# Kernel optimization log

Hardware: AMD Instinct MI355X
Metric: run time of the kernel (lower is better)

The kernel has to match this reference:

```python
import jax, jax.numpy as jnp
import numpy as np

HIDDEN = 512
SR = 16000
MAX_MSGS = 512
EOT = 2.0  # END_OF_TRACK message-type id (round-to-nearest-even match, like Python round)


def gru_cell(x, h, w_ih, w_hh, b_ih, b_hh):
    # PyTorch GRU cell equations
    gi = w_ih @ x + b_ih          # [3H]
    gh = w_hh @ h + b_hh          # [3H]
    i_r, i_z, i_n = jnp.split(gi, 3)
    h_r, h_z, h_n = jnp.split(gh, 3)
    r = jax.nn.sigmoid(i_r + h_r)
    z = jax.nn.sigmoid(i_z + h_z)
    n = jnp.tanh(i_n + r * h_n)
    return (1.0 - z) * n + z * h


def setup_inputs() -> dict:
    key = jax.random.key(0)
    ks = jax.random.split(key, 8)
    s = 0.02  # keep gates unsaturated
    return {
        "x": jax.random.normal(ks[0], (1, 32, SR), dtype=jnp.float32),
        "enc_w_ih": jax.random.normal(ks[1], (3 * HIDDEN, SR), jnp.float32) * s,
        "enc_w_hh": jax.random.normal(ks[2], (3 * HIDDEN, HIDDEN), jnp.float32) * s,
        "enc_b_ih": jnp.zeros((3 * HIDDEN,), jnp.float32),
        "enc_b_hh": jnp.zeros((3 * HIDDEN,), jnp.float32),
        "dec_w_ih": jax.random.normal(ks[3], (3 * HIDDEN, 6), jnp.float32) * s,
        "dec_w_hh": jax.random.normal(ks[4], (3 * HIDDEN, HIDDEN), jnp.float32) * s,
        "dec_b_ih": jnp.zeros((3 * HIDDEN,), jnp.float32),
        "dec_b_hh": jnp.zeros((3 * HIDDEN,), jnp.float32),
        "lin_w": jax.random.normal(ks[5], (6, HIDDEN), jnp.float32) * s,
        "lin_b": jnp.zeros((6,), jnp.float32),
    }


def _forward(x, enc_w_ih, enc_w_hh, enc_b_ih, enc_b_hh,
             dec_w_ih, dec_w_hh, dec_b_ih, dec_b_hh, lin_w, lin_b):
    # --- encoder: hidden_states[0] in the torch code is the final hidden of
    # encoder layer 0, forward direction (other layers/direction never reach the output).
    xs = x[0]  # [T, SR], batch_size == 1 (required by the original indexing)

    def enc_step(h, xt):
        return gru_cell(xt, h, enc_w_ih, enc_w_hh, enc_b_ih, enc_b_hh), None

    h_enc, _ = jax.lax.scan(enc_step, jnp.zeros((HIDDEN,), x.dtype), xs)

    # --- decoder step 0: zero input, init hidden = h_enc
    h = gru_cell(jnp.zeros((6,), x.dtype), h_enc, dec_w_ih, dec_w_hh, dec_b_ih, dec_b_hh)
    msg0 = lin_w @ h + lin_b
    midi = jnp.zeros((MAX_MSGS, 6), x.dtype).at[0].set(msg0)
    # NOTE: the original never writes midi[:,1] (off-by-one: messages jumps 1 -> 2);
    # torch leaves uninitialized garbage there, we leave zeros.

    def dec_step(carry, _):
        midi, h, last, messages, active = carry
        cond = active & (jnp.round(last[0]) != EOT) & (messages < MAX_MSGS - 1)
        h_new = gru_cell(last, h, dec_w_ih, dec_w_hh, dec_b_ih, dec_b_hh)
        msg = lin_w @ h_new + lin_b
        messages = jnp.where(cond, messages + 1, messages)
        h = jnp.where(cond, h_new, h)
        midi = midi.at[messages].set(jnp.where(cond, msg, midi[messages]))
        last = jnp.where(cond, msg, last)
        return (midi, h, last, messages, cond), None

    init = (midi, h, msg0, jnp.array(1, jnp.int32), jnp.array(True))
    (midi, _, _, messages, _), _ = jax.lax.scan(dec_step, init, None, length=MAX_MSGS - 2)
    num_messages = (messages + 1)[None].astype(jnp.int32)  # torch uses uint32
    return midi[None], num_messages  # ([1, MAX_MSGS, 6], [1])


def reference(x, enc_w_ih, enc_w_hh, enc_b_ih, enc_b_hh,
              dec_w_ih, dec_w_hh, dec_b_ih, dec_b_hh, lin_w, lin_b):
    return _forward(x, enc_w_ih, enc_w_hh, enc_b_ih, enc_b_hh,
                    dec_w_ih, dec_w_hh, dec_b_ih, dec_b_hh, lin_w, lin_b)
```

## Files before the change

kernel.cpp:

```cpp
#include <hip/hip_runtime.h>


#define HID 512
#define G3  1536
#define NWG 16
#define TPB 384
#define JPW 32
#define RPW 96

#define WS_CNT  0
#define WS_HEX  64
#define WS_PMSG 1088
#define WS_GI   4096

__device__ __forceinline__ float sigmf(float x) { return 1.0f / (1.0f + expf(-x)); }

__device__ __forceinline__ void st_agent(float* p, float v) {
  __hip_atomic_store((unsigned int*)p, __float_as_uint(v), __ATOMIC_RELAXED, __HIP_MEMORY_SCOPE_AGENT);
}
__device__ __forceinline__ float ld_agent(const float* p) {
  unsigned int u = __hip_atomic_load((const unsigned int*)p, __ATOMIC_RELAXED, __HIP_MEMORY_SCOPE_AGENT);
  return __uint_as_float(u);
}
__device__ __forceinline__ void ld_agent2(const float* p, float& a, float& b) {
  unsigned long long u = __hip_atomic_load((const unsigned long long*)p, __ATOMIC_RELAXED, __HIP_MEMORY_SCOPE_AGENT);
  a = __uint_as_float((unsigned int)u);
  b = __uint_as_float((unsigned int)(u >> 32));
}

__global__ __launch_bounds__(256) void k0_init(float* __restrict__ ws, float* __restrict__ out,
                                               const float* __restrict__ enc_b_ih) {
  int i = blockIdx.x * 256 + threadIdx.x;
  int n = gridDim.x * 256;
  for (int j = i; j < 4096; j += n) ws[j] = 0.0f;
  for (int j = i; j < 32 * G3; j += n) ws[WS_GI + j] = enc_b_ih[j % G3];
  for (int j = i; j < 3073; j += n) out[j] = 0.0f;
}

#define KB 160
__global__ __launch_bounds__(256) void k1_gemm(const float* __restrict__ x,
                                               const float* __restrict__ wih,
                                               float* __restrict__ ws) {
  __shared__ float lw[64][KB + 4];
  __shared__ float lx[32][KB + 4];
  const int m0  = blockIdx.x * 64;
  const int k00 = blockIdx.y * 1600;
  const int t   = threadIdx.x;
  const int rg  = t >> 4;
  const int tg  = t & 15;
  float acc[4][2] = {{0.f,0.f},{0.f,0.f},{0.f,0.f},{0.f,0.f}};
  for (int c = 0; c < 10; ++c) {
    const int kc = k00 + c * KB;
    __syncthreads();
    #pragma unroll
    for (int j = 0; j < 10; ++j) {
      int idx = t + j * 256;
      int r = idx / 40, c4 = idx % 40;
      float4 v = *reinterpret_cast<const float4*>(wih + (long)(m0 + r) * 16000 + kc + c4 * 4);
      *reinterpret_cast<float4*>(&lw[r][c4 * 4]) = v;
    }
    #pragma unroll
    for (int j = 0; j < 5; ++j) {
      int idx = t + j * 256;
      int r = idx / 40, c4 = idx % 40;
      float4 v = *reinterpret_cast<const float4*>(x + (long)r * 16000 + kc + c4 * 4);
      *reinterpret_cast<float4*>(&lx[r][c4 * 4]) = v;
    }
    __syncthreads();
    for (int kk = 0; kk < KB; kk += 4) {
      float4 xv0 = *reinterpret_cast<const float4*>(&lx[tg * 2 + 0][kk]);
      float4 xv1 = *reinterpret_cast<const float4*>(&lx[tg * 2 + 1][kk]);
      #pragma unroll
      for (int j = 0; j < 4; ++j) {
        float4 wv = *reinterpret_cast<const float4*>(&lw[rg * 4 + j][kk]);
        acc[j][0] += wv.x * xv0.x + wv.y * xv0.y + wv.z * xv0.z + wv.w * xv0.w;
        acc[j][1] += wv.x * xv1.x + wv.y * xv1.y + wv.z * xv1.z + wv.w * xv1.w;
      }
    }
  }
  #pragma unroll
  for (int j = 0; j < 4; ++j)
    #pragma unroll
    for (int u = 0; u < 2; ++u)
      atomicAdd(&ws[WS_GI + (tg * 2 + u) * G3 + m0 + rg * 4 + j], acc[j][u]);
}

__device__ __forceinline__ void load_wslice(const float* __restrict__ whh, int j0, int rg, int cg,
                                            float w[8][16]) {
  #pragma unroll
  for (int k = 0; k < 8; ++k) {
    const int lr = rg * 8 + k;
    const int grow = (lr >> 5) * HID + j0 + (lr & 31);
    const float* src = whh + grow * HID + cg * 16;
    #pragma unroll
    for (int q = 0; q < 4; ++q) {
      float4 v = *reinterpret_cast<const float4*>(src + q * 4);
      w[k][q * 4 + 0] = v.x; w[k][q * 4 + 1] = v.y;
      w[k][q * 4 + 2] = v.z; w[k][q * 4 + 3] = v.w;
    }
  }
}

__global__ __launch_bounds__(TPB) void k2_rnn(
    const float* __restrict__ enc_w_hh, const float* __restrict__ enc_b_hh,
    const float* __restrict__ dec_w_ih, const float* __restrict__ dec_w_hh,
    const float* __restrict__ dec_b_ih, const float* __restrict__ dec_b_hh,
    const float* __restrict__ lin_w, const float* __restrict__ lin_b,
    float* __restrict__ ws, float* __restrict__ out) {
  __shared__ float gsum[RPW];
  __shared__ float h_own[JPW];
  __shared__ float s_last[8];
  __shared__ float s_wih[RPW][6];
  __shared__ float s_bih[RPW];
  __shared__ float s_bhh[RPW];
  __shared__ float s_linw[6][JPW];
  __shared__ float s_linb[6];
  __shared__ float s_pm[NWG][6];

  const int wg = blockIdx.x;
  const int t  = threadIdx.x;
  const int rg = t >> 5;
  const int cg = t & 31;
  const int j0 = wg * JPW;

  unsigned* cnt = (unsigned*)ws;
  float* hex  = ws + WS_HEX;
  float* pmsg = ws + WS_PMSG;
  const float* gi_enc = ws + WS_GI;

  float w[8][16];
  unsigned bstep = 0;
  int p = 0;

  load_wslice(enc_w_hh, j0, rg, cg, w);
  if (t < RPW) {
    const int grow = (t >> 5) * HID + j0 + (t & 31);
    s_bhh[t] = enc_b_hh[grow];
  }
  if (t < JPW) h_own[t] = 0.0f;
  __syncthreads();

  for (int s = 0; s < 32; ++s) {
    float hr[16];
    {
      const float* hb = hex + p * HID + cg * 16;
      #pragma unroll
      for (int u = 0; u < 8; ++u) ld_agent2(hb + 2 * u, hr[2 * u], hr[2 * u + 1]);
    }
    float gi0 = 0.f, gi1 = 0.f, gi2 = 0.f;
    if (t < JPW) {
      const float* g = gi_enc + s * G3 + j0 + t;
      gi0 = g[0]; gi1 = g[HID]; gi2 = g[2 * HID];
    }
    float acc[8];
    #pragma unroll
    for (int k = 0; k < 8; ++k) {
      float a = 0.f;
      #pragma unroll
      for (int i = 0; i < 16; ++i) a = fmaf(w[k][i], hr[i], a);
      acc[k] = a;
    }
    #pragma unroll
    for (int m = 1; m <= 16; m <<= 1) {
      #pragma unroll
      for (int k = 0; k < 8; ++k) acc[k] += __shfl_xor(acc[k], m, 64);
    }
    if (cg == 0) {
      #pragma unroll
      for (int k = 0; k < 8; ++k) gsum[rg * 8 + k] = acc[k];
    }
    __syncthreads();
    if (t < JPW) {
      float r = sigmf(gi0 + gsum[t]      + s_bhh[t]);
      float z = sigmf(gi1 + gsum[32 + t] + s_bhh[32 + t]);
      float n = tanhf(gi2 + r * (gsum[64 + t] + s_bhh[64 + t]));
      float hn = (1.0f - z) * n + z * h_own[t];
      h_own[t] = hn;
      st_agent(&hex[(p ^ 1) * HID + j0 + t], hn);
    }
    p ^= 1;
    ++bstep;
    __syncthreads();
    if (t == 0) {
      __hip_atomic_fetch_add(cnt, 1u, __ATOMIC_ACQ_REL, __HIP_MEMORY_SCOPE_AGENT);
      const unsigned tgt = NWG * bstep;
      while (__hip_atomic_load(cnt, __ATOMIC_ACQUIRE, __HIP_MEMORY_SCOPE_AGENT) < tgt)
        __builtin_amdgcn_s_sleep(1);
    }
    __syncthreads();
  }

  load_wslice(dec_w_hh, j0, rg, cg, w);
  if (t < RPW) {
    const int grow = (t >> 5) * HID + j0 + (t & 31);
    s_bih[t] = dec_b_ih[grow];
    s_bhh[t] = dec_b_hh[grow];
    #pragma unroll
    for (int m = 0; m < 6; ++m) s_wih[t][m] = dec_w_ih[grow * 6 + m];
  }
  if (t < 192) {
    const int m = t >> 5, jj = t & 31;
    s_linw[m][jj] = lin_w[m * HID + j0 + jj];
  }
  if (t < 6) s_linb[t] = lin_b[t];
  __syncthreads();

  int messages = 1;

  for (int k = 0; k <= 510; ++k) {
    if (k >= 1) {
      const bool cond = (rintf(s_last[0]) != 2.0f) && (messages < 511);
      if (!cond) break;
    }
    float hr[16];
    {
      const float* hb = hex + p * HID + cg * 16;
      #pragma unroll
      for (int u = 0; u < 8; ++u) ld_agent2(hb + 2 * u, hr[2 * u], hr[2 * u + 1]);
    }
    float acc[8];
    #pragma unroll
    for (int kk = 0; kk < 8; ++kk) {
      float a = 0.f;
      #pragma unroll
      for (int i = 0; i < 16; ++i) a = fmaf(w[kk][i], hr[i], a);
      acc[kk] = a;
    }
    #pragma unroll
    for (int m = 1; m <= 16; m <<= 1) {
      #pragma unroll
      for (int kk = 0; kk < 8; ++kk) acc[kk] += __shfl_xor(acc[kk], m, 64);
    }
    if (cg == 0) {
      #pragma unroll
      for (int kk = 0; kk < 8; ++kk) gsum[rg * 8 + kk] = acc[kk];
    }
    __syncthreads();
    if (t < JPW) {
      float gi0 = s_bih[t], gi1 = s_bih[32 + t], gi2 = s_bih[64 + t];
      if (k >= 1) {
        #pragma unroll
        for (int m = 0; m < 6; ++m) {
          gi0 = fmaf(s_wih[t][m],      s_last[m], gi0);
          gi1 = fmaf(s_wih[32 + t][m], s_last[m], gi1);
          gi2 = fmaf(s_wih[64 + t][m], s_last[m], gi2);
        }
      }
      float r = sigmf(gi0 + gsum[t]      + s_bhh[t]);
      float z = sigmf(gi1 + gsum[32 + t] + s_bhh[32 + t]);
      float n = tanhf(gi2 + r * (gsum[64 + t] + s_bhh[64 + t]));
      float hn = (1.0f - z) * n + z * h_own[t];
      h_own[t] = hn;
      st_agent(&hex[(p ^ 1) * HID + j0 + t], hn);
    }
    __syncthreads();
    if (t >= 32 && t < 38) {
      const int m = t - 32;
      float pm = 0.f;
      #pragma unroll
      for (int jj = 0; jj < JPW; ++jj) pm = fmaf(s_linw[m][jj], h_own[jj], pm);
      st_agent(&pmsg[(k & 1) * NWG * 8 + wg * 8 + m], pm);
    }
    p ^= 1;
    ++bstep;
    __syncthreads();
    if (t == 0) {
      __hip_atomic_fetch_add(cnt, 1u, __ATOMIC_ACQ_REL, __HIP_MEMORY_SCOPE_AGENT);
      const unsigned tgt = NWG * bstep;
      while (__hip_atomic_load(cnt, __ATOMIC_ACQUIRE, __HIP_MEMORY_SCOPE_AGENT) < tgt)
        __builtin_amdgcn_s_sleep(1);
    }
    __syncthreads();
    if (t >= 128 && t < 128 + NWG * 6) {
      const int wi = (t - 128) / 6, m = (t - 128) % 6;
      s_pm[wi][m] = ld_agent(&pmsg[(k & 1) * NWG * 8 + wi * 8 + m]);
    }
    __syncthreads();
    if (t < 6) {
      float sme = s_linb[t];
      #pragma unroll
      for (int wi = 0; wi < NWG; ++wi) sme += s_pm[wi][t];
      s_last[t] = sme;
      if (wg == 0) {
        const int row = (k == 0) ? 0 : (messages + 1);
        out[row * 6 + t] = sme;
      }
    }
    __syncthreads();
    if (k >= 1) ++messages;
  }

  if (wg == 0 && t == 0) out[3072] = (float)(messages + 1);
}

extern "C" void kernel_launch(void* const* d_in, const int* in_sizes, int n_in,
                              void* d_out, int out_size, void* d_ws, size_t ws_size,
                              hipStream_t stream) {
  const float* x        = (const float*)d_in[0];
  const float* enc_w_ih = (const float*)d_in[1];
  const float* enc_w_hh = (const float*)d_in[2];
  const float* enc_b_ih = (const float*)d_in[3];
  const float* enc_b_hh = (const float*)d_in[4];
  const float* dec_w_ih = (const float*)d_in[5];
  const float* dec_w_hh = (const float*)d_in[6];
  const float* dec_b_ih = (const float*)d_in[7];
  const float* dec_b_hh = (const float*)d_in[8];
  const float* lin_w    = (const float*)d_in[9];
  const float* lin_b    = (const float*)d_in[10];
  float* ws  = (float*)d_ws;
  float* out = (float*)d_out;

  hipLaunchKernelGGL(k0_init, dim3(64), dim3(256), 0, stream, ws, out, enc_b_ih);
  hipLaunchKernelGGL(k1_gemm, dim3(24, 10), dim3(256), 0, stream, x, enc_w_ih, ws);
  hipLaunchKernelGGL(k2_rnn, dim3(NWG), dim3(TPB), 0, stream,
                     enc_w_hh, enc_b_hh, dec_w_ih, dec_w_hh, dec_b_ih, dec_b_hh,
                     lin_w, lin_b, ws, out);
}
```

Baseline: 2.269 ms.

## Replace atomic counter barrier with per-workgroup stamps and fuse message reduction

The global barrier moves from a single fetch-add counter to per-workgroup release stamps on separate cache lines, with 16 threads each polling one stamp. The decoder's linear-output partial sum becomes a wave shuffle reduction done by the gate threads, and the cross-workgroup message sum is done by shuffles right after the barrier, which removes several __syncthreads and shared-memory round trips per step. Hidden state is kept in a register instead of shared memory. The intent is to cut per-step synchronisation latency in the serial recurrence. The cost is more polling traffic from many readers, and the workspace layout shifts, so the init kernel must zero the new stamp region.

```diff
diff --git a/kernel.cpp b/kernel.cpp
--- a/kernel.cpp
+++ b/kernel.cpp
@@ -8,10 +8,10 @@
 #define JPW 32
 #define RPW 96
 
-#define WS_CNT  0
-#define WS_HEX  64
-#define WS_PMSG 1088
-#define WS_GI   4096
+#define WS_STAMP 0
+#define WS_HEX   512
+#define WS_PMSG  1536
+#define WS_GI    4096
 
 __device__ __forceinline__ float sigmf(float x) { return 1.0f / (1.0f + expf(-x)); }
 
@@ -101,21 +101,19 @@
   }
 }
 
-__global__ __launch_bounds__(TPB) void k2_rnn(
+__global__ __launch_bounds__(TPB, 1) void k2_rnn(
     const float* __restrict__ enc_w_hh, const float* __restrict__ enc_b_hh,
     const float* __restrict__ dec_w_ih, const float* __restrict__ dec_w_hh,
     const float* __restrict__ dec_b_ih, const float* __restrict__ dec_b_hh,
     const float* __restrict__ lin_w, const float* __restrict__ lin_b,
     float* __restrict__ ws, float* __restrict__ out) {
   __shared__ float gsum[RPW];
-  __shared__ float h_own[JPW];
   __shared__ float s_last[8];
   __shared__ float s_wih[RPW][6];
   __shared__ float s_bih[RPW];
   __shared__ float s_bhh[RPW];
   __shared__ float s_linw[6][JPW];
-  __shared__ float s_linb[6];
-  __shared__ float s_pm[NWG][6];
+  __shared__ float s_linb[8];
 
   const int wg = blockIdx.x;
   const int t  = threadIdx.x;
@@ -123,12 +121,13 @@
   const int cg = t & 31;
   const int j0 = wg * JPW;
 
-  unsigned* cnt = (unsigned*)ws;
+  unsigned* stamp = (unsigned*)ws;
   float* hex  = ws + WS_HEX;
   float* pmsg = ws + WS_PMSG;
   const float* gi_enc = ws + WS_GI;
 
   float w[8][16];
+  float hreg = 0.0f;
   unsigned bstep = 0;
   int p = 0;
 
@@ -137,7 +136,6 @@
     const int grow = (t >> 5) * HID + j0 + (t & 31);
     s_bhh[t] = enc_b_hh[grow];
   }
-  if (t < JPW) h_own[t] = 0.0f;
   __syncthreads();
 
   for (int s = 0; s < 32; ++s) {
@@ -147,47 +145,43 @@
       #pragma unroll
       for (int u = 0; u < 8; ++u) ld_agent2(hb + 2 * u, hr[2 * u], hr[2 * u + 1]);
     }
-    float gi0 = 0.f, gi1 = 0.f, gi2 = 0.f;
+    float acc[8];
+    #pragma unroll
+    for (int kk = 0; kk < 8; ++kk) {
+      float a = 0.f;
+      #pragma unroll
+      for (int i = 0; i < 16; ++i) a = fmaf(w[kk][i], hr[i], a);
+      acc[kk] = a;
+    }
+    #pragma unroll
+    for (int m = 1; m <= 16; m <<= 1) {
+      #pragma unroll
+      for (int kk = 0; kk < 8; ++kk) acc[kk] += __shfl_xor(acc[kk], m, 64);
+    }
+    if (cg == 0) {
+      #pragma unroll
+      for (int kk = 0; kk < 8; ++kk) gsum[rg * 8 + kk] = acc[kk];
+    }
+    __syncthreads();
     if (t < JPW) {
       const float* g = gi_enc + s * G3 + j0 + t;
-      gi0 = g[0]; gi1 = g[HID]; gi2 = g[2 * HID];
-    }
-    float acc[8];
-    #pragma unroll
-    for (int k = 0; k < 8; ++k) {
-      float a = 0.f;
-      #pragma unroll
-      for (int i = 0; i < 16; ++i) a = fmaf(w[k][i], hr[i], a);
-      acc[k] = a;
-    }
-    #pragma unroll
-    for (int m = 1; m <= 16; m <<= 1) {
-      #pragma unroll
-      for (int k = 0; k < 8; ++k) acc[k] += __shfl_xor(acc[k], m, 64);
-    }
-    if (cg == 0) {
-      #pragma unroll
-      for (int k = 0; k < 8; ++k) gsum[rg * 8 + k] = acc[k];
-    }
-    __syncthreads();
-    if (t < JPW) {
-      float r = sigmf(gi0 + gsum[t]      + s_bhh[t]);
-      float z = sigmf(gi1 + gsum[32 + t] + s_bhh[32 + t]);
-      float n = tanhf(gi2 + r * (gsum[64 + t] + s_bhh[64 + t]));
-      float hn = (1.0f - z) * n + z * h_own[t];
-      h_own[t] = hn;
+      float r = sigmf(g[0]       + gsum[t]      + s_bhh[t]);
+      float z = sigmf(g[HID]     + gsum[32 + t] + s_bhh[32 + t]);
+      float n = tanhf(g[2 * HID] + r * (gsum[64 + t] + s_bhh[64 + t]));
+      float hn = (1.0f - z) * n + z * hreg;
+      hreg = hn;
       st_agent(&hex[(p ^ 1) * HID + j0 + t], hn);
     }
+    __syncthreads();
+    if (t == 0)
+      __hip_atomic_store(&stamp[wg * 32], bstep + 1, __ATOMIC_RELEASE, __HIP_MEMORY_SCOPE_AGENT);
+    ++bstep;
+    if (t < NWG) {
+      while (__hip_atomic_load(&stamp[t * 32], __ATOMIC_ACQUIRE, __HIP_MEMORY_SCOPE_AGENT) < bstep)
+        __builtin_amdgcn_s_sleep(1);
+    }
+    __syncthreads();
     p ^= 1;
-    ++bstep;
-    __syncthreads();
-    if (t == 0) {
-      __hip_atomic_fetch_add(cnt, 1u, __ATOMIC_ACQ_REL, __HIP_MEMORY_SCOPE_AGENT);
-      const unsigned tgt = NWG * bstep;
-      while (__hip_atomic_load(cnt, __ATOMIC_ACQUIRE, __HIP_MEMORY_SCOPE_AGENT) < tgt)
-        __builtin_amdgcn_s_sleep(1);
-    }
-    __syncthreads();
   }
 
   load_wslice(dec_w_hh, j0, rg, cg, w);
@@ -249,44 +243,51 @@
       float r = sigmf(gi0 + gsum[t]      + s_bhh[t]);
       float z = sigmf(gi1 + gsum[32 + t] + s_bhh[32 + t]);
       float n = tanhf(gi2 + r * (gsum[64 + t] + s_bhh[64 + t]));
-      float hn = (1.0f - z) * n + z * h_own[t];
-      h_own[t] = hn;
+      float hn = (1.0f - z) * n + z * hreg;
+      hreg = hn;
       st_agent(&hex[(p ^ 1) * HID + j0 + t], hn);
-    }
-    __syncthreads();
-    if (t >= 32 && t < 38) {
-      const int m = t - 32;
-      float pm = 0.f;
-      #pragma unroll
-      for (int jj = 0; jj < JPW; ++jj) pm = fmaf(s_linw[m][jj], h_own[jj], pm);
-      st_agent(&pmsg[(k & 1) * NWG * 8 + wg * 8 + m], pm);
-    }
+      float c0 = s_linw[0][t] * hn, c1 = s_linw[1][t] * hn, c2 = s_linw[2][t] * hn;
+      float c3 = s_linw[3][t] * hn, c4 = s_linw[4][t] * hn, c5 = s_linw[5][t] * hn;
+      #pragma unroll
+      for (int m = 1; m <= 16; m <<= 1) {
+        c0 += __shfl_xor(c0, m, 64); c1 += __shfl_xor(c1, m, 64); c2 += __shfl_xor(c2, m, 64);
+        c3 += __shfl_xor(c3, m, 64); c4 += __shfl_xor(c4, m, 64); c5 += __shfl_xor(c5, m, 64);
+      }
+      if (t == 0) {
+        float* pm = pmsg + (k & 1) * NWG * 8 + wg * 8;
+        st_agent(pm + 0, c0); st_agent(pm + 1, c1); st_agent(pm + 2, c2);
+        st_agent(pm + 3, c3); st_agent(pm + 4, c4); st_agent(pm + 5, c5);
+      }
+    }
+    __syncthreads();
+    if (t == 0)
+      __hip_atomic_store(&stamp[wg * 32], bstep + 1, __ATOMIC_RELEASE, __HIP_MEMORY_SCOPE_AGENT);
+    ++bstep;
+    if (t < NWG) {
+      while (__hip_atomic_load(&stamp[t * 32], __ATOMIC_ACQUIRE, __HIP_MEMORY_SCOPE_AGENT) < bstep)
+        __builtin_amdgcn_s_sleep(1);
+      const float* pm = pmsg + (k & 1) * NWG * 8 + t * 8;
+      float g0 = ld_agent(pm + 0), g1 = ld_agent(pm + 1), g2 = ld_agent(pm + 2);
+      float g3 = ld_agent(pm + 3), g4 = ld_agent(pm + 4), g5 = ld_agent(pm + 5);
+      #pragma unroll
+      for (int m = 1; m <= 8; m <<= 1) {
+        g0 += __shfl_xor(g0, m, 64); g1 += __shfl_xor(g1, m, 64); g2 += __shfl_xor(g2, m, 64);
+        g3 += __shfl_xor(g3, m, 64); g4 += __shfl_xor(g4, m, 64); g5 += __shfl_xor(g5, m, 64);
+      }
+      if (t == 0) {
+        g0 += s_linb[0]; g1 += s_linb[1]; g2 += s_linb[2];
+        g3 += s_linb[3]; g4 += s_linb[4]; g5 += s_linb[5];
+        s_last[0] = g0; s_last[1] = g1; s_last[2] = g2;
+        s_last[3] = g3; s_last[4] = g4; s_last[5] = g5;
+        if (wg == 0) {
+          const int row = (k == 0) ? 0 : (messages + 1);
+          float* o = out + row * 6;
+          o[0] = g0; o[1] = g1; o[2] = g2; o[3] = g3; o[4] = g4; o[5] = g5;
+        }
+      }
+    }
+    __syncthreads();
     p ^= 1;
-    ++bstep;
-    __syncthreads();
-    if (t == 0) {
-      __hip_atomic_fetch_add(cnt, 1u, __ATOMIC_ACQ_REL, __HIP_MEMORY_SCOPE_AGENT);
-      const unsigned tgt = NWG * bstep;
-      while (__hip_atomic_load(cnt, __ATOMIC_ACQUIRE, __HIP_MEMORY_SCOPE_AGENT) < tgt)
-        __builtin_amdgcn_s_sleep(1);
-    }
-    __syncthreads();
-    if (t >= 128 && t < 128 + NWG * 6) {
-      const int wi = (t - 128) / 6, m = (t - 128) % 6;
-      s_pm[wi][m] = ld_agent(&pmsg[(k & 1) * NWG * 8 + wi * 8 + m]);
-    }
-    __syncthreads();
-    if (t < 6) {
-      float sme = s_linb[t];
-      #pragma unroll
-      for (int wi = 0; wi < NWG; ++wi) sme += s_pm[wi][t];
-      s_last[t] = sme;
-      if (wg == 0) {
-        const int row = (k == 0) ? 0 : (messages + 1);
-        out[row * 6 + t] = sme;
-      }
-    }
-    __syncthreads();
     if (k >= 1) ++messages;
   }
 
```

After: 2.556 ms. 12.7% more time.

## Replace grid barrier with tagged-value flag sync and specialize gate wave

Applied to the files above, without the earlier changes.

Drops the atomic-counter grid barrier. Each hidden value and partial message is now published as a 64-bit word holding a step tag and the float, and consumers poll until the tags match. The block is split into 12 matvec waves and one gate/output wave that double-buffer through shared memory, so the output reduction is folded into the per-step publish. The init kernel also touches both recurrent weight matrices to warm the L2 cache, and fast exp replaces expf/tanhf. The risks are that the tagged-slot workspace is no longer zeroed, so stale tags from earlier runs could be matched, and that the fast exp is less accurate.

```diff
diff --git a/kernel.cpp b/kernel.cpp
--- a/kernel.cpp
+++ b/kernel.cpp
@@ -4,37 +4,40 @@
 #define HID 512
 #define G3  1536
 #define NWG 16
-#define TPB 384
+#define TPB 832
 #define JPW 32
-#define RPW 96
-
-#define WS_CNT  0
-#define WS_HEX  64
-#define WS_PMSG 1088
+
+typedef unsigned long long u64;
+typedef unsigned int u32;
+
 #define WS_GI   4096
-
-__device__ __forceinline__ float sigmf(float x) { return 1.0f / (1.0f + expf(-x)); }
-
-__device__ __forceinline__ void st_agent(float* p, float v) {
-  __hip_atomic_store((unsigned int*)p, __float_as_uint(v), __ATOMIC_RELAXED, __HIP_MEMORY_SCOPE_AGENT);
-}
-__device__ __forceinline__ float ld_agent(const float* p) {
-  unsigned int u = __hip_atomic_load((const unsigned int*)p, __ATOMIC_RELAXED, __HIP_MEMORY_SCOPE_AGENT);
-  return __uint_as_float(u);
-}
-__device__ __forceinline__ void ld_agent2(const float* p, float& a, float& b) {
-  unsigned long long u = __hip_atomic_load((const unsigned long long*)p, __ATOMIC_RELAXED, __HIP_MEMORY_SCOPE_AGENT);
-  a = __uint_as_float((unsigned int)u);
-  b = __uint_as_float((unsigned int)(u >> 32));
+#define WS_SINK 3800
+
+__device__ __forceinline__ float sigmf(float x) { return 1.0f / (1.0f + __expf(-x)); }
+
+__device__ __forceinline__ u64 ld64(const u64* p) {
+  return __hip_atomic_load(p, __ATOMIC_RELAXED, __HIP_MEMORY_SCOPE_AGENT);
+}
+__device__ __forceinline__ void st64(u64* p, u64 v) {
+  __hip_atomic_store(p, v, __ATOMIC_RELAXED, __HIP_MEMORY_SCOPE_AGENT);
 }
 
 __global__ __launch_bounds__(256) void k0_init(float* __restrict__ ws, float* __restrict__ out,
-                                               const float* __restrict__ enc_b_ih) {
+                                               const float* __restrict__ enc_b_ih,
+                                               const float* __restrict__ enc_w_hh,
+                                               const float* __restrict__ dec_w_hh) {
   int i = blockIdx.x * 256 + threadIdx.x;
   int n = gridDim.x * 256;
-  for (int j = i; j < 4096; j += n) ws[j] = 0.0f;
+  for (int j = i; j < 3073; j += n) out[j] = 0.0f;
   for (int j = i; j < 32 * G3; j += n) ws[WS_GI + j] = enc_b_ih[j % G3];
-  for (int j = i; j < 3073; j += n) out[j] = 0.0f;
+  float s = 0.f;
+  const float4* a = (const float4*)enc_w_hh;
+  const float4* b = (const float4*)dec_w_hh;
+  for (int j = i; j < G3 * HID / 4; j += n) {
+    float4 u = a[j], v = b[j];
+    s += u.x + u.y + u.z + u.w + v.x + v.y + v.z + v.w;
+  }
+  if (s == 1234567.8f) ws[WS_SINK] = s;
 }
 
 #define KB 160
@@ -85,212 +88,293 @@
       atomicAdd(&ws[WS_GI + (tg * 2 + u) * G3 + m0 + rg * 4 + j], acc[j][u]);
 }
 
-__device__ __forceinline__ void load_wslice(const float* __restrict__ whh, int j0, int rg, int cg,
-                                            float w[8][16]) {
+__device__ __forceinline__ void load_w(const float* __restrict__ whh, int j0, int rg, int cg,
+                                       float w[8][8]) {
   #pragma unroll
-  for (int k = 0; k < 8; ++k) {
-    const int lr = rg * 8 + k;
-    const int grow = (lr >> 5) * HID + j0 + (lr & 31);
-    const float* src = whh + grow * HID + cg * 16;
-    #pragma unroll
-    for (int q = 0; q < 4; ++q) {
-      float4 v = *reinterpret_cast<const float4*>(src + q * 4);
-      w[k][q * 4 + 0] = v.x; w[k][q * 4 + 1] = v.y;
-      w[k][q * 4 + 2] = v.z; w[k][q * 4 + 3] = v.w;
-    }
+  for (int i2 = 0; i2 < 8; ++i2) {
+    const int r = rg * 8 + i2;
+    const int grow = (r >> 5) * HID + j0 + (r & 31);
+    const float* src = whh + grow * HID + cg;
+    #pragma unroll
+    for (int u = 0; u < 8; ++u) w[i2][u] = src[64 * u];
   }
 }
 
-__global__ __launch_bounds__(TPB) void k2_rnn(
+__device__ __forceinline__ bool poll_h(const u64* hb, u32 want, float hr[8],
+                                       const int* brk_p, bool escape) {
+  u64 v[8];
+  #pragma unroll
+  for (int u = 0; u < 8; ++u) v[u] = ld64(hb + 64 * u);
+  for (;;) {
+    bool all = true;
+    #pragma unroll
+    for (int u = 0; u < 8; ++u) all = all && ((u32)(v[u] >> 32) == want);
+    if (all) break;
+    if (escape && __hip_atomic_load(brk_p, __ATOMIC_RELAXED, __HIP_MEMORY_SCOPE_WORKGROUP))
+      return true;
+    __builtin_amdgcn_s_sleep(1);
+    #pragma unroll
+    for (int u = 0; u < 8; ++u)
+      if ((u32)(v[u] >> 32) != want) v[u] = ld64(hb + 64 * u);
+  }
+  #pragma unroll
+  for (int u = 0; u < 8; ++u) hr[u] = __uint_as_float((u32)v[u]);
+  return false;
+}
+
+__global__ __launch_bounds__(TPB, 1) void k2_rnn(
     const float* __restrict__ enc_w_hh, const float* __restrict__ enc_b_hh,
     const float* __restrict__ dec_w_ih, const float* __restrict__ dec_w_hh,
     const float* __restrict__ dec_b_ih, const float* __restrict__ dec_b_hh,
     const float* __restrict__ lin_w, const float* __restrict__ lin_b,
     float* __restrict__ ws, float* __restrict__ out) {
-  __shared__ float gsum[RPW];
-  __shared__ float h_own[JPW];
-  __shared__ float s_last[8];
-  __shared__ float s_wih[RPW][6];
-  __shared__ float s_bih[RPW];
-  __shared__ float s_bhh[RPW];
-  __shared__ float s_linw[6][JPW];
-  __shared__ float s_linb[6];
-  __shared__ float s_pm[NWG][6];
+  __shared__ float gsum[2][96];
+  __shared__ int s_brk;
 
   const int wg = blockIdx.x;
   const int t  = threadIdx.x;
-  const int rg = t >> 5;
-  const int cg = t & 31;
   const int j0 = wg * JPW;
 
-  unsigned* cnt = (unsigned*)ws;
-  float* hex  = ws + WS_HEX;
-  float* pmsg = ws + WS_PMSG;
+  u64* hexT = (u64*)ws;
+  u64* pmT  = hexT + 1024;
   const float* gi_enc = ws + WS_GI;
 
-  float w[8][16];
-  unsigned bstep = 0;
-  int p = 0;
-
-  load_wslice(enc_w_hh, j0, rg, cg, w);
-  if (t < RPW) {
-    const int grow = (t >> 5) * HID + j0 + (t & 31);
-    s_bhh[t] = enc_b_hh[grow];
+  if (t < 768) {
+    const int rg = t >> 6;
+    const int cg = t & 63;
+    float w[8][8];
+    load_w(enc_w_hh, j0, rg, cg, w);
+
+    for (int s = 0; s < 32; ++s) {
+      float hr[8];
+      if (s == 0) {
+        #pragma unroll
+        for (int u = 0; u < 8; ++u) hr[u] = 0.f;
+      } else {
+        const u32 want = (u32)s;
+        poll_h(hexT + (want & 1) * 512 + cg, want, hr, &s_brk, false);
+      }
+      float acc[8];
+      #pragma unroll
+      for (int i2 = 0; i2 < 8; ++i2) {
+        float a = 0.f;
+        #pragma unroll
+        for (int u = 0; u < 8; ++u) a = fmaf(w[i2][u], hr[u], a);
+        acc[i2] = a;
+      }
+      #pragma unroll
+      for (int m = 1; m <= 32; m <<= 1) {
+        #pragma unroll
+        for (int i2 = 0; i2 < 8; ++i2) acc[i2] += __shfl_xor(acc[i2], m, 64);
+      }
+      if (cg == 0) {
+        #pragma unroll
+        for (int i2 = 0; i2 < 8; ++i2) gsum[s & 1][rg * 8 + i2] = acc[i2];
+      }
+      __syncthreads();
+    }
+
+    load_w(dec_w_hh, j0, rg, cg, w);
+    __syncthreads();
+
+    for (int k = 0; k <= 510; ++k) {
+      const u32 want = 32u + (u32)k;
+      float hr[8];
+      if (poll_h(hexT + (want & 1) * 512 + cg, want, hr, &s_brk, true)) break;
+      float acc[8];
+      #pragma unroll
+      for (int i2 = 0; i2 < 8; ++i2) {
+        float a = 0.f;
+        #pragma unroll
+        for (int u = 0; u < 8; ++u) a = fmaf(w[i2][u], hr[u], a);
+        acc[i2] = a;
+      }
+      #pragma unroll
+      for (int m = 1; m <= 32; m <<= 1) {
+        #pragma unroll
+        for (int i2 = 0; i2 < 8; ++i2) acc[i2] += __shfl_xor(acc[i2], m, 64);
+      }
+      if (cg == 0) {
+        #pragma unroll
+        for (int i2 = 0; i2 < 8; ++i2) gsum[k & 1][rg * 8 + i2] = acc[i2];
+      }
+      __syncthreads();
+    }
+  } else {
+    const int lane = t - 768;
+    float hreg = 0.f;
+    float eb0 = 0, eb1 = 0, eb2 = 0;
+    if (lane < 32) {
+      eb0 = enc_b_hh[j0 + lane];
+      eb1 = enc_b_hh[HID + j0 + lane];
+      eb2 = enc_b_hh[2 * HID + j0 + lane];
+    }
+    for (int s = 0; s < 32; ++s) {
+      float gi0 = 0, gi1 = 0, gi2 = 0;
+      if (lane < 32) {
+        const float* g = gi_enc + s * G3 + j0 + lane;
+        gi0 = g[0]; gi1 = g[HID]; gi2 = g[2 * HID];
+      }
+      __syncthreads();
+      if (lane < 32) {
+        const float* gs = gsum[s & 1];
+        float rr = sigmf(gi0 + gs[lane] + eb0);
+        float zz = sigmf(gi1 + gs[32 + lane] + eb1);
+        float ee = __expf(-2.f * (gi2 + rr * (gs[64 + lane] + eb2)));
+        float nn = (1.f - ee) / (1.f + ee);
+        hreg = (1.f - zz) * nn + zz * hreg;
+        const u32 tg = (u32)s + 1u;
+        st64(&hexT[(tg & 1) * 512 + j0 + lane], ((u64)tg << 32) | (u64)__float_as_uint(hreg));
+      }
+    }
+    float di0 = 0, di1 = 0, di2 = 0, dh0 = 0, dh1 = 0, dh2 = 0;
+    float wr[6], wz[6], wn[6], lw[6], lb[6];
+    #pragma unroll
+    for (int m = 0; m < 6; ++m) { wr[m]=0; wz[m]=0; wn[m]=0; lw[m]=0; lb[m]=0; }
+    if (lane < 32) {
+      const int jr = j0 + lane;
+      di0 = dec_b_ih[jr]; di1 = dec_b_ih[HID + jr]; di2 = dec_b_ih[2 * HID + jr];
+      dh0 = dec_b_hh[jr]; dh1 = dec_b_hh[HID + jr]; dh2 = dec_b_hh[2 * HID + jr];
+      #pragma unroll
+      for (int m = 0; m < 6; ++m) {
+        wr[m] = dec_w_ih[jr * 6 + m];
+        wz[m] = dec_w_ih[(HID + jr) * 6 + m];
+        wn[m] = dec_w_ih[(2 * HID + jr) * 6 + m];
+        lw[m] = lin_w[m * HID + jr];
+      }
+    }
+    if (lane >= 32 && lane < 48) {
+      #pragma unroll
+      for (int m = 0; m < 6; ++m) lb[m] = lin_b[m];
+    }
+    if (lane == 32) s_brk = 0;
+    __syncthreads();
+
+    int messages = 1, pendrow = 0;
+    bool pend = false, alive = true;
+
+    for (int k = 0; k <= 510 && alive; ++k) {
+      float m0 = 0, m1 = 0, m2 = 0, m3 = 0, m4 = 0, m5 = 0;
+      bool cond = true;
+      if (k >= 1) {
+        const u32 want = 32u + (u32)k;
+        float g0 = 0, g1 = 0, g2 = 0, g3 = 0, g4 = 0, g5 = 0;
+        if (lane >= 32 && lane < 48) {
+          const u64* pb = pmT + (want & 1) * 128 + (lane - 32) * 8;
+          u64 v[6];
+          #pragma unroll
+          for (int m = 0; m < 6; ++m) v[m] = ld64(pb + m);
+          for (;;) {
+            bool all = true;
+            #pragma unroll
+            for (int m = 0; m < 6; ++m) all = all && ((u32)(v[m] >> 32) == want);
+            if (all) break;
+            __builtin_amdgcn_s_sleep(1);
+            #pragma unroll
+            for (int m = 0; m < 6; ++m)
+              if ((u32)(v[m] >> 32) != want) v[m] = ld64(pb + m);
+          }
+          g0 = __uint_as_float((u32)v[0]); g1 = __uint_as_float((u32)v[1]);
+          g2 = __uint_as_float((u32)v[2]); g3 = __uint_as_float((u32)v[3]);
+          g4 = __uint_as_float((u32)v[4]); g5 = __uint_as_float((u32)v[5]);
+          #pragma unroll
+          for (int mm = 1; mm <= 8; mm <<= 1) {
+            g0 += __shfl_xor(g0, mm, 64); g1 += __shfl_xor(g1, mm, 64);
+            g2 += __shfl_xor(g2, mm, 64); g3 += __shfl_xor(g3, mm, 64);
+            g4 += __shfl_xor(g4, mm, 64); g5 += __shfl_xor(g5, mm, 64);
+          }
+          g0 += lb[0]; g1 += lb[1]; g2 += lb[2]; g3 += lb[3]; g4 += lb[4]; g5 += lb[5];
+        }
+        m0 = __shfl(g0, 32, 64); m1 = __shfl(g1, 32, 64); m2 = __shfl(g2, 32, 64);
+        m3 = __shfl(g3, 32, 64); m4 = __shfl(g4, 32, 64); m5 = __shfl(g5, 32, 64);
+        if (pend && wg == 0 && lane == 32) {
+          float* o = out + pendrow * 6;
+          o[0] = m0; o[1] = m1; o[2] = m2; o[3] = m3; o[4] = m4; o[5] = m5;
+        }
+        cond = (rintf(m0) != 2.0f) && (messages < 511);
+      }
+      __syncthreads();
+      if (cond) {
+        if (lane < 32) {
+          float gi0 = di0, gi1 = di1, gi2 = di2;
+          if (k >= 1) {
+            gi0 += wr[0]*m0 + wr[1]*m1 + wr[2]*m2 + wr[3]*m3 + wr[4]*m4 + wr[5]*m5;
+            gi1 += wz[0]*m0 + wz[1]*m1 + wz[2]*m2 + wz[3]*m3 + wz[4]*m4 + wz[5]*m5;
+            gi2 += wn[0]*m0 + wn[1]*m1 + wn[2]*m2 + wn[3]*m3 + wn[4]*m4 + wn[5]*m5;
+          }
+          const float* gs = gsum[k & 1];
+          float rr = sigmf(gi0 + gs[lane] + dh0);
+          float zz = sigmf(gi1 + gs[32 + lane] + dh1);
+          float ee = __expf(-2.f * (gi2 + rr * (gs[64 + lane] + dh2)));
+          float nn = (1.f - ee) / (1.f + ee);
+          hreg = (1.f - zz) * nn + zz * hreg;
+          const u32 tg = 33u + (u32)k;
+          st64(&hexT[(tg & 1) * 512 + j0 + lane], ((u64)tg << 32) | (u64)__float_as_uint(hreg));
+          float c0 = lw[0]*hreg, c1 = lw[1]*hreg, c2 = lw[2]*hreg;
+          float c3 = lw[3]*hreg, c4 = lw[4]*hreg, c5 = lw[5]*hreg;
+          #pragma unroll
+          for (int mm = 1; mm <= 16; mm <<= 1) {
+            c0 += __shfl_xor(c0, mm, 64); c1 += __shfl_xor(c1, mm, 64);
+            c2 += __shfl_xor(c2, mm, 64); c3 += __shfl_xor(c3, mm, 64);
+            c4 += __shfl_xor(c4, mm, 64); c5 += __shfl_xor(c5, mm, 64);
+          }
+          if (lane == 0) {
+            u64* pb = pmT + (tg & 1) * 128 + wg * 8;
+            st64(pb + 0, ((u64)tg << 32) | (u64)__float_as_uint(c0));
+            st64(pb + 1, ((u64)tg << 32) | (u64)__float_as_uint(c1));
+            st64(pb + 2, ((u64)tg << 32) | (u64)__float_as_uint(c2));
+            st64(pb + 3, ((u64)tg << 32) | (u64)__float_as_uint(c3));
+            st64(pb + 4, ((u64)tg << 32) | (u64)__float_as_uint(c4));
+            st64(pb + 5, ((u64)tg << 32) | (u64)__float_as_uint(c5));
+          }
+        }
+        if (k >= 1) ++messages;
+        pendrow = (k == 0) ? 0 : messages;
+        pend = true;
+      } else {
+        if (lane == 32)
+          __hip_atomic_store(&s_brk, 1, __ATOMIC_RELAXED, __HIP_MEMORY_SCOPE_WORKGROUP);
+        pend = false;
+        alive = false;
+      }
+    }
+
+    if (pend && wg == 0) {
+      const u32 want = 543u;
+      float g0 = 0, g1 = 0, g2 = 0, g3 = 0, g4 = 0, g5 = 0;
+      if (lane >= 32 && lane < 48) {
+        const u64* pb = pmT + (want & 1) * 128 + (lane - 32) * 8;
+        u64 v[6];
+        #pragma unroll
+        for (int m = 0; m < 6; ++m) v[m] = ld64(pb + m);
+        for (;;) {
+          bool all = true;
+          #pragma unroll
+          for (int m = 0; m < 6; ++m) all = all && ((u32)(v[m] >> 32) == want);
+          if (all) break;
+          __builtin_amdgcn_s_sleep(1);
+          #pragma unroll
+          for (int m = 0; m < 6; ++m)
+            if ((u32)(v[m] >> 32) != want) v[m] = ld64(pb + m);
+        }
+        g0 = __uint_as_float((u32)v[0]); g1 = __uint_as_float((u32)v[1]);
+        g2 = __uint_as_float((u32)v[2]); g3 = __uint_as_float((u32)v[3]);
+        g4 = __uint_as_float((u32)v[4]); g5 = __uint_as_float((u32)v[5]);
+        #pragma unroll
+        for (int mm = 1; mm <= 8; mm <<= 1) {
+          g0 += __shfl_xor(g0, mm, 64); g1 += __shfl_xor(g1, mm, 64);
+          g2 += __shfl_xor(g2, mm, 64); g3 += __shfl_xor(g3, mm, 64);
+          g4 += __shfl_xor(g4, mm, 64); g5 += __shfl_xor(g5, mm, 64);
+        }
+        g0 += lb[0]; g1 += lb[1]; g2 += lb[2]; g3 += lb[3]; g4 += lb[4]; g5 += lb[5];
+        if (lane == 32) {
+          float* o = out + pendrow * 6;
+          o[0] = g0; o[1] = g1; o[2] = g2; o[3] = g3; o[4] = g4; o[5] = g5;
+        }
+      }
+    }
+    if (wg == 0 && lane == 32) out[3072] = (float)(messages + 1);
   }
-  if (t < JPW) h_own[t] = 0.0f;
-  __syncthreads();
-
-  for (int s = 0; s < 32; ++s) {
-    float hr[16];
-    {
-      const float* hb = hex + p * HID + cg * 16;
-      #pragma unroll
-      for (int u = 0; u < 8; ++u) ld_agent2(hb + 2 * u, hr[2 * u], hr[2 * u + 1]);
-    }
-    float gi0 = 0.f, gi1 = 0.f, gi2 = 0.f;
-    if (t < JPW) {
-      const float* g = gi_enc + s * G3 + j0 + t;
-      gi0 = g[0]; gi1 = g[HID]; gi2 = g[2 * HID];
-    }
-    float acc[8];
-    #pragma unroll
-    for (int k = 0; k < 8; ++k) {
-      float a = 0.f;
-      #pragma unroll
-      for (int i = 0; i < 16; ++i) a = fmaf(w[k][i], hr[i], a);
-      acc[k] = a;
-    }
-    #pragma unroll
-    for (int m = 1; m <= 16; m <<= 1) {
-      #pragma unroll
-      for (int k = 0; k < 8; ++k) acc[k] += __shfl_xor(acc[k], m, 64);
-    }
-    if (cg == 0) {
-      #pragma unroll
-      for (int k = 0; k < 8; ++k) gsum[rg * 8 + k] = acc[k];
-    }
-    __syncthreads();
-    if (t < JPW) {
-      float r = sigmf(gi0 + gsum[t]      + s_bhh[t]);
-      float z = sigmf(gi1 + gsum[32 + t] + s_bhh[32 + t]);
-      float n = tanhf(gi2 + r * (gsum[64 + t] + s_bhh[64 + t]));
-      float hn = (1.0f - z) * n + z * h_own[t];
-      h_own[t] = hn;
-      st_agent(&hex[(p ^ 1) * HID + j0 + t], hn);
-    }
-    p ^= 1;
-    ++bstep;
-    __syncthreads();
-    if (t == 0) {
-      __hip_atomic_fetch_add(cnt, 1u, __ATOMIC_ACQ_REL, __HIP_MEMORY_SCOPE_AGENT);
-      const unsigned tgt = NWG * bstep;
-      while (__hip_atomic_load(cnt, __ATOMIC_ACQUIRE, __HIP_MEMORY_SCOPE_AGENT) < tgt)
-        __builtin_amdgcn_s_sleep(1);
-    }
-    __syncthreads();
-  }
-
-  load_wslice(dec_w_hh, j0, rg, cg, w);
-  if (t < RPW) {
-    const int grow = (t >> 5) * HID + j0 + (t & 31);
-    s_bih[t] = dec_b_ih[grow];
-    s_bhh[t] = dec_b_hh[grow];
-    #pragma unroll
-    for (int m = 0; m < 6; ++m) s_wih[t][m] = dec_w_ih[grow * 6 + m];
-  }
-  if (t < 192) {
-    const int m = t >> 5, jj = t & 31;
-    s_linw[m][jj] = lin_w[m * HID + j0 + jj];
-  }
-  if (t < 6) s_linb[t] = lin_b[t];
-  __syncthreads();
-
-  int messages = 1;
-
-  for (int k = 0; k <= 510; ++k) {
-    if (k >= 1) {
-      const bool cond = (rintf(s_last[0]) != 2.0f) && (messages < 511);
-      if (!cond) break;
-    }
-    float hr[16];
-    {
-      const float* hb = hex + p * HID + cg * 16;
-      #pragma unroll
-      for (int u = 0; u < 8; ++u) ld_agent2(hb + 2 * u, hr[2 * u], hr[2 * u + 1]);
-    }
-    float acc[8];
-    #pragma unroll
-    for (int kk = 0; kk < 8; ++kk) {
-      float a = 0.f;
-      #pragma unroll
-      for (int i = 0; i < 16; ++i) a = fmaf(w[kk][i], hr[i], a);
-      acc[kk] = a;
-    }
-    #pragma unroll
-    for (int m = 1; m <= 16; m <<= 1) {
-      #pragma unroll
-      for (int kk = 0; kk < 8; ++kk) acc[kk] += __shfl_xor(acc[kk], m, 64);
-    }
-    if (cg == 0) {
-      #pragma unroll
-      for (int kk = 0; kk < 8; ++kk) gsum[rg * 8 + kk] = acc[kk];
-    }
-    __syncthreads();
-    if (t < JPW) {
-      float gi0 = s_bih[t], gi1 = s_bih[32 + t], gi2 = s_bih[64 + t];
-      if (k >= 1) {
-        #pragma unroll
-        for (int m = 0; m < 6; ++m) {
-          gi0 = fmaf(s_wih[t][m],      s_last[m], gi0);
-          gi1 = fmaf(s_wih[32 + t][m], s_last[m], gi1);
-          gi2 = fmaf(s_wih[64 + t][m], s_last[m], gi2);
-        }
-      }
-      float r = sigmf(gi0 + gsum[t]      + s_bhh[t]);
-      float z = sigmf(gi1 + gsum[32 + t] + s_bhh[32 + t]);
-      float n = tanhf(gi2 + r * (gsum[64 + t] + s_bhh[64 + t]));
-      float hn = (1.0f - z) * n + z * h_own[t];
-      h_own[t] = hn;
-      st_agent(&hex[(p ^ 1) * HID + j0 + t], hn);
-    }
-    __syncthreads();
-    if (t >= 32 && t < 38) {
-      const int m = t - 32;
-      float pm = 0.f;
-      #pragma unroll
-      for (int jj = 0; jj < JPW; ++jj) pm = fmaf(s_linw[m][jj], h_own[jj], pm);
-      st_agent(&pmsg[(k & 1) * NWG * 8 + wg * 8 + m], pm);
-    }
-    p ^= 1;
-    ++bstep;
-    __syncthreads();
-    if (t == 0) {
-      __hip_atomic_fetch_add(cnt, 1u, __ATOMIC_ACQ_REL, __HIP_MEMORY_SCOPE_AGENT);
-      const unsigned tgt = NWG * bstep;
-      while (__hip_atomic_load(cnt, __ATOMIC_ACQUIRE, __HIP_MEMORY_SCOPE_AGENT) < tgt)
-        __builtin_amdgcn_s_sleep(1);
-    }
-    __syncthreads();
-    if (t >= 128 && t < 128 + NWG * 6) {
-      const int wi = (t - 128) / 6, m = (t - 128) % 6;
-      s_pm[wi][m] = ld_agent(&pmsg[(k & 1) * NWG * 8 + wi * 8 + m]);
-    }
-    __syncthreads();
-    if (t < 6) {
-      float sme = s_linb[t];
-      #pragma unroll
-      for (int wi = 0; wi < NWG; ++wi) sme += s_pm[wi][t];
-      s_last[t] = sme;
-      if (wg == 0) {
-        const int row = (k == 0) ? 0 : (messages + 1);
-        out[row * 6 + t] = sme;
-      }
-    }
-    __syncthreads();
-    if (k >= 1) ++messages;
-  }
-
-  if (wg == 0 && t == 0) out[3072] = (float)(messages + 1);
 }
 
 extern "C" void kernel_launch(void* const* d_in, const int* in_sizes, int n_in,
@@ -310,7 +394,7 @@
   float* ws  = (float*)d_ws;
   float* out = (float*)d_out;
 
-  hipLaunchKernelGGL(k0_init, dim3(64), dim3(256), 0, stream, ws, out, enc_b_ih);
+  hipLaunchKernelGGL(k0_init, dim3(64), dim3(256), 0, stream, ws, out, enc_b_ih, enc_w_hh, dec_w_hh);
   hipLaunchKernelGGL(k1_gemm, dim3(24, 10), dim3(256), 0, stream, x, enc_w_ih, ws);
   hipLaunchKernelGGL(k2_rnn, dim3(NWG), dim3(TPB), 0, stream,
                      enc_w_hh, enc_b_hh, dec_w_ih, dec_w_hh, dec_b_ih, dec_b_hh,
```

Result: slower. 2.793 ms (+23.1%).
